# Optimization experiments

Hardware: AMD Instinct MI355X
Metric: run time of the kernel (lower is better)

Reference implementation:

```python
import jax, jax.numpy as jnp
import numpy as np

B, T, C = 2, 2048, 1024
H, D = 16, 64


def setup_inputs() -> dict:
    key = jax.random.key(0)
    ks = jax.random.split(key, 5)
    s = 1.0 / np.sqrt(C)  # keep projections well-scaled
    return {
        "x": jax.random.normal(ks[0], (B, T, C), dtype=jnp.float32),
        "wq": jax.random.normal(ks[1], (C, C), dtype=jnp.float32) * s,
        "wk": jax.random.normal(ks[2], (C, C), dtype=jnp.float32) * s,
        "wv": jax.random.normal(ks[3], (C, C), dtype=jnp.float32) * s,
        "wo": jax.random.normal(ks[4], (C, C), dtype=jnp.float32) * s,
    }


def reference(x, wq, wk, wv, wo):
    # nn.Linear(d,d,bias=False): y = x @ W.T ; weights stored [out,in]
    q = (x @ wq.T).reshape(B, T, H, D).transpose(0, 2, 1, 3)  # [B,H,T,D]
    k = (x @ wk.T).reshape(B, T, H, D).transpose(0, 2, 1, 3)
    v = (x @ wv.T).reshape(B, T, H, D).transpose(0, 2, 1, 3)
    scale = jnp.sqrt(jnp.float32(D))
    scores = jnp.einsum("bhtd,bhsd->bhts", q, k) / scale  # [B,H,T,T]
    # additive causal mask: -inf above the diagonal
    causal = jnp.tril(jnp.ones((T, T), dtype=bool))
    scores = jnp.where(causal[None, None], scores, jnp.float32(-1e9))
    weights = jax.nn.softmax(scores, axis=-1)
    out = jnp.einsum("bhts,bhsd->bhtd", weights, v)  # [B,H,T,D]
    out = out.transpose(0, 2, 1, 3).reshape(B, T, C)
    return out @ wo.T
```

## Files before the change

kernel.cpp:

```cpp
#include <hip/hip_runtime.h>
#include <stdint.h>

#define B_ 2
#define T_ 2048
#define C_ 1024
#define H_ 16
#define D_ 64
#define M_ (B_*T_)

typedef __attribute__((ext_vector_type(8))) short bf16x8;
typedef __attribute__((ext_vector_type(4))) short bf16x4;
typedef __attribute__((ext_vector_type(4))) float f32x4;
typedef unsigned short u16;

#define MFMA32(a, b, c) __builtin_amdgcn_mfma_f32_16x16x32_bf16((a), (b), (c), 0, 0, 0)
#if defined(__HIP_DEVICE_COMPILE__)
# if __has_builtin(__builtin_amdgcn_mfma_f32_16x16x16bf16_1k)
#  define MFMA16(a, b, c) __builtin_amdgcn_mfma_f32_16x16x16bf16_1k((a), (b), (c), 0, 0, 0)
# else
#  define MFMA16(a, b, c) __builtin_amdgcn_mfma_f32_16x16x16_bf16((a), (b), (c), 0, 0, 0)
# endif
#else
# define MFMA16(a, b, c) (c)
#endif

__device__ __forceinline__ u16 f2bf(float f) {
  union { float f; uint32_t u; } v; v.f = f;
  uint32_t u = v.u;
  return (u16)((u + 0x7fffu + ((u >> 16) & 1u)) >> 16);
}

__device__ __forceinline__ float exp2_fast(float x) { return __builtin_amdgcn_exp2f(x); }

typedef const __attribute__((address_space(1))) void* gas_t;
typedef __attribute__((address_space(3))) void* las_t;
__device__ __forceinline__ void gld_lds16(const void* g, void* l) {
  __builtin_amdgcn_global_load_lds((gas_t)g, (las_t)l, 16, 0, 0);
}

__global__ void cvt_bf16(const float* __restrict__ src, u16* __restrict__ dst) {
  int i = (blockIdx.x * blockDim.x + threadIdx.x) * 4;
  float4 v = *(const float4*)(src + i);
  ushort4 o;
  o.x = f2bf(v.x); o.y = f2bf(v.y); o.z = f2bf(v.z); o.w = f2bf(v.w);
  *(ushort4*)(dst + i) = o;
}

__global__ void cvt_bf16_w4(const float* __restrict__ s0, const float* __restrict__ s1,
                            const float* __restrict__ s2, const float* __restrict__ s3,
                            u16* __restrict__ d0, u16* __restrict__ d1,
                            u16* __restrict__ d2, u16* __restrict__ d3) {
  const float* s; u16* d;
  switch (blockIdx.y) {
    case 0: s = s0; d = d0; break;
    case 1: s = s1; d = d1; break;
    case 2: s = s2; d = d2; break;
    default: s = s3; d = d3; break;
  }
  int i = (blockIdx.x * blockDim.x + threadIdx.x) * 4;
  float4 v = *(const float4*)(s + i);
  ushort4 o;
  o.x = f2bf(v.x); o.y = f2bf(v.y); o.z = f2bf(v.z); o.w = f2bf(v.w);
  *(ushort4*)(d + i) = o;
}

__device__ __forceinline__ void gemm_core(const u16* __restrict__ A,
                                          const u16* __restrict__ W,
                                          int m0, int n0, int Kt,
                                          f32x4 acc[4][4])
{
  __shared__ u16 As[128*64];
  __shared__ u16 Bs[128*64];
  const int t = threadIdx.x;
  const int lane = t & 63;
  const int wave = t >> 6;
  const int q = lane >> 4;
  const int l15 = lane & 15;
  const int wm = (wave >> 1) * 64;
  const int wn = (wave & 1) * 64;

  #pragma unroll
  for (int i = 0; i < 4; ++i)
    #pragma unroll
    for (int j = 0; j < 4; ++j)
      acc[i][j] = (f32x4){0.f, 0.f, 0.f, 0.f};

  for (int k0 = 0; k0 < Kt; k0 += 64) {
    #pragma unroll
    for (int r = 0; r < 4; ++r) {
      int Lc = r * 256 + t;
      int row = Lc >> 3;
      int gcc = (Lc & 7) ^ (row & 7);
      gld_lds16(A + (size_t)(m0 + row) * Kt + k0 + gcc * 8, As + Lc * 8);
    }
    #pragma unroll
    for (int r = 0; r < 4; ++r) {
      int Lc = r * 256 + t;
      int row = Lc >> 3;
      int gcc = (Lc & 7) ^ (row & 7);
      gld_lds16(W + (size_t)(n0 + row) * Kt + k0 + gcc * 8, Bs + Lc * 8);
    }
    __syncthreads();

    #pragma unroll
    for (int kk = 0; kk < 2; ++kk) {
      bf16x8 af[4], bfr[4];
      #pragma unroll
      for (int i = 0; i < 4; ++i) {
        int m = wm + i * 16 + l15;
        int ch = (kk * 4 + q) ^ (m & 7);
        af[i] = *(const bf16x8*)(As + m * 64 + ch * 8);
      }
      #pragma unroll
      for (int j = 0; j < 4; ++j) {
        int n = wn + j * 16 + l15;
        int ch = (kk * 4 + q) ^ (n & 7);
        bfr[j] = *(const bf16x8*)(Bs + n * 64 + ch * 8);
      }
      #pragma unroll
      for (int i = 0; i < 4; ++i)
        #pragma unroll
        for (int j = 0; j < 4; ++j)
          acc[i][j] = MFMA32(af[i], bfr[j], acc[i][j]);
    }
    __syncthreads();
  }
}

#define QSCALE 0.1803368801111244f
__global__ __launch_bounds__(256, 3)
void gemm_qkv(const u16* __restrict__ X,
              const u16* __restrict__ Wq, const u16* __restrict__ Wk,
              const u16* __restrict__ Wv,
              u16* __restrict__ Q, u16* __restrict__ K, u16* __restrict__ Vt)
{
  const int bm = blockIdx.x;
  const int bn = blockIdx.y;
  const int seg = bn >> 3;
  const int n0 = (bn & 7) * 128;
  const u16* W = (seg == 0) ? Wq : ((seg == 1) ? Wk : Wv);

  f32x4 acc[4][4];
  gemm_core(X, W, bm * 128, n0, C_, acc);

  const int t = threadIdx.x, lane = t & 63, wave = t >> 6;
  const int q = lane >> 4, l15 = lane & 15;
  const int wm = (wave >> 1) * 64, wn = (wave & 1) * 64;
  const float scale = (seg == 0) ? QSCALE : 1.0f;

  #pragma unroll
  for (int i = 0; i < 4; ++i) {
    #pragma unroll
    for (int j = 0; j < 4; ++j) {
      const int mbase = bm * 128 + wm + i * 16 + q * 4;
      const int n = n0 + wn + j * 16 + l15;
      const int h = n >> 6, d = n & 63;
      if (seg < 2) {
        u16* dst = (seg == 0) ? Q : K;
        #pragma unroll
        for (int r = 0; r < 4; ++r) {
          const int m = mbase + r;
          const int b = m >> 11, tt = m & (T_ - 1);
          size_t idx = (((size_t)(b * H_ + h)) * T_ + tt) * D_ + d;
          dst[idx] = f2bf(acc[i][j][r] * scale);
        }
      } else {
        const int b = mbase >> 11, tt = mbase & (T_ - 1);
        size_t idx = (((size_t)(b * H_ + h)) * D_ + d) * T_ + tt;
        ushort4 pk;
        pk.x = f2bf(acc[i][j][0]); pk.y = f2bf(acc[i][j][1]);
        pk.z = f2bf(acc[i][j][2]); pk.w = f2bf(acc[i][j][3]);
        *(ushort4*)(Vt + idx) = pk;
      }
    }
  }
}

__global__ __launch_bounds__(256, 2)
void attn(const u16* __restrict__ Q, const u16* __restrict__ K,
          const u16* __restrict__ Vt, u16* __restrict__ Att)
{
  __shared__ u16 Ks[2][64 * 64];
  __shared__ u16 Vs[2][64 * 64];
  const int t = threadIdx.x;
  const int lane = t & 63, wave = t >> 6;
  const int q = lane >> 4, l15 = lane & 15;
  const int pr = blockIdx.x;
  const int bh = blockIdx.y;
  const int qbA = pr * 64;
  const int qbB = (31 - pr) * 64;
  const u16* Qp = Q + (size_t)bh * T_ * D_;
  const u16* Kp = K + (size_t)bh * T_ * D_;
  const u16* Vp = Vt + (size_t)bh * D_ * T_;

  const int rowA = qbA + 4 * l15 + wave;
  const int rowB = qbB + 4 * l15 + wave;
  const u16* qra = Qp + (size_t)rowA * 64;
  const u16* qrb = Qp + (size_t)rowB * 64;
  const bf16x8 aqA0 = *(const bf16x8*)(qra + q * 8);
  const bf16x8 aqA1 = *(const bf16x8*)(qra + 32 + q * 8);
  const bf16x8 aqB0 = *(const bf16x8*)(qrb + q * 8);
  const bf16x8 aqB1 = *(const bf16x8*)(qrb + 32 + q * 8);

  f32x4 oA[4], oB[4];
  #pragma unroll
  for (int j = 0; j < 4; ++j) {
    oA[j] = (f32x4){0.f, 0.f, 0.f, 0.f};
    oB[j] = (f32x4){0.f, 0.f, 0.f, 0.f};
  }
  float lsA = 0.f, lsB = 0.f;

  auto stage = [&](int kb, int buf) {
    #pragma unroll
    for (int r = 0; r < 2; ++r) {
      int c = r * 256 + t, row = c >> 3, gcc = (c & 7) ^ (row & 7);
      gld_lds16(Kp + (size_t)(kb + row) * 64 + gcc * 8, &Ks[buf][c * 8]);
    }
    #pragma unroll
    for (int r = 0; r < 2; ++r) {
      int c = r * 256 + t, row = c >> 3, gcc = (c & 7) ^ (row & 7);
      gld_lds16(Vp + (size_t)row * T_ + kb + gcc * 8, &Vs[buf][c * 8]);
    }
  };

  stage(0, 0);
  int cur = 0;
  for (int kb = 0; kb <= qbB; kb += 64, cur ^= 1) {
    __syncthreads();
    if (kb + 64 <= qbB) stage(kb + 64, cur ^ 1);
    const u16* Kc = &Ks[cur][0];
    const u16* Vc = &Vs[cur][0];

    bf16x8 kf0[4], kf1[4];
    #pragma unroll
    for (int j2 = 0; j2 < 4; ++j2) {
      const int row = j2 * 16 + l15;
      kf0[j2] = *(const bf16x8*)(Kc + row * 64 + ((q)     ^ (row & 7)) * 8);
      kf1[j2] = *(const bf16x8*)(Kc + row * 64 + ((4 + q) ^ (row & 7)) * 8);
    }
    bf16x4 vf[4][4];
    #pragma unroll
    for (int j = 0; j < 4; ++j) {
      const int row = j * 16 + l15;
      #pragma unroll
      for (int j2 = 0; j2 < 4; ++j2) {
        const int ch = (2 * j2 + (q >> 1)) ^ (row & 7);
        vf[j][j2] = *(const bf16x4*)(Vc + row * 64 + ch * 8 + (q & 1) * 4);
      }
    }

    auto tile_compute = [&](const bf16x8 a0, const bf16x8 a1, f32x4* o,
                            float& lsum, int rowg, bool diag) {
      bf16x4 pb[4];
      #pragma unroll
      for (int j2 = 0; j2 < 4; ++j2) {
        f32x4 z = (f32x4){0.f, 0.f, 0.f, 0.f};
        z = MFMA32(kf0[j2], a0, z);
        z = MFMA32(kf1[j2], a1, z);
        if (diag) {
          #pragma unroll
          for (int r = 0; r < 4; ++r) {
            const int key = kb + j2 * 16 + q * 4 + r;
            if (key > rowg) z[r] = -1e30f;
          }
        }
        float p0 = exp2_fast(z[0]), p1 = exp2_fast(z[1]);
        float p2 = exp2_fast(z[2]), p3 = exp2_fast(z[3]);
        lsum += (p0 + p1) + (p2 + p3);
        pb[j2] = (bf16x4){(short)f2bf(p0), (short)f2bf(p1),
                          (short)f2bf(p2), (short)f2bf(p3)};
      }
      #pragma unroll
      for (int j = 0; j < 4; ++j)
        #pragma unroll
        for (int j2 = 0; j2 < 4; ++j2)
          o[j] = MFMA16(vf[j][j2], pb[j2], o[j]);
    };

    tile_compute(aqB0, aqB1, oB, lsB, rowB, kb == qbB);
    if (kb <= qbA)
      tile_compute(aqA0, aqA1, oA, lsA, rowA, kb == qbA);
  }

  lsA += __shfl_xor(lsA, 16, 64); lsA += __shfl_xor(lsA, 32, 64);
  lsB += __shfl_xor(lsB, 16, 64); lsB += __shfl_xor(lsB, 32, 64);
  const float invA = __builtin_amdgcn_rcpf(lsA);
  const float invB = __builtin_amdgcn_rcpf(lsB);

  const int b = bh >> 4, h = bh & 15;
  #pragma unroll
  for (int j = 0; j < 4; ++j) {
    ushort4 pa, pbk;
    pa.x = f2bf(oA[j][0] * invA); pa.y = f2bf(oA[j][1] * invA);
    pa.z = f2bf(oA[j][2] * invA); pa.w = f2bf(oA[j][3] * invA);
    pbk.x = f2bf(oB[j][0] * invB); pbk.y = f2bf(oB[j][1] * invB);
    pbk.z = f2bf(oB[j][2] * invB); pbk.w = f2bf(oB[j][3] * invB);
    *(ushort4*)(Att + ((size_t)b * T_ + rowA) * C_ + h * 64 + j * 16 + q * 4) = pa;
    *(ushort4*)(Att + ((size_t)b * T_ + rowB) * C_ + h * 64 + j * 16 + q * 4) = pbk;
  }
}

__global__ __launch_bounds__(256, 3)
void gemm_out(const u16* __restrict__ Att, const u16* __restrict__ Wo,
              float* __restrict__ Out)
{
  const int bm = blockIdx.x, bn = blockIdx.y;
  f32x4 acc[4][4];
  gemm_core(Att, Wo, bm * 128, bn * 128, C_, acc);

  const int t = threadIdx.x, lane = t & 63, wave = t >> 6;
  const int q = lane >> 4, l15 = lane & 15;
  const int wm = (wave >> 1) * 64, wn = (wave & 1) * 64;

  #pragma unroll
  for (int i = 0; i < 4; ++i) {
    #pragma unroll
    for (int j = 0; j < 4; ++j) {
      const int m0 = bm * 128 + wm + i * 16 + q * 4;
      const int n = bn * 128 + wn + j * 16 + l15;
      #pragma unroll
      for (int r = 0; r < 4; ++r)
        Out[(size_t)(m0 + r) * C_ + n] = acc[i][j][r];
    }
  }
}

extern "C" void kernel_launch(void* const* d_in, const int* in_sizes, int n_in,
                              void* d_out, int out_size, void* d_ws, size_t ws_size,
                              hipStream_t stream) {
  const float* x  = (const float*)d_in[0];
  const float* wq = (const float*)d_in[1];
  const float* wk = (const float*)d_in[2];
  const float* wv = (const float*)d_in[3];
  const float* wo = (const float*)d_in[4];
  float* out = (float*)d_out;

  u16* ws  = (u16*)d_ws;
  u16* xb  = ws;
  u16* wqb = xb  + (size_t)M_ * C_;
  u16* wkb = wqb + (size_t)C_ * C_;
  u16* wvb = wkb + (size_t)C_ * C_;
  u16* wob = wvb + (size_t)C_ * C_;
  u16* Qb  = wob + (size_t)C_ * C_;
  u16* Kb  = Qb  + (size_t)M_ * C_;
  u16* Vtb = Kb  + (size_t)M_ * C_;
  u16* Atb = Vtb + (size_t)M_ * C_;

  cvt_bf16<<<dim3(M_ * C_ / 1024), 256, 0, stream>>>(x, xb);
  cvt_bf16_w4<<<dim3(C_ * C_ / 1024, 4), 256, 0, stream>>>(wq, wk, wv, wo,
                                                           wqb, wkb, wvb, wob);

  gemm_qkv<<<dim3(M_ / 128, 24), 256, 0, stream>>>(xb, wqb, wkb, wvb, Qb, Kb, Vtb);
  attn<<<dim3(16, B_ * H_), 256, 0, stream>>>(Qb, Kb, Vtb, Atb);
  gemm_out<<<dim3(M_ / 128, C_ / 128), 256, 0, stream>>>(Atb, wob, out);
}
```

Before: 176.8 us.

## Use 16x16x32 MFMA for PV via permuted V layout; retile output GEMM

The QKV GEMM now writes V transposed with a permuted token order inside each 32-token group. This lets the attention kernel load V as bf16x8 fragments and compute P·V with the 16x16x32 bf16 MFMA instead of pairs of 16x16x16 MFMAs, halving the PV instruction count and the number of LDS reads. The output projection gets its own kernel with 64x128 tiles, giving twice as many blocks so the GPU is better filled. That kernel is single-buffered, with a barrier on every k-step, which may expose load latency.

```diff
diff --git a/kernel.cpp b/kernel.cpp
--- a/kernel.cpp
+++ b/kernel.cpp
@@ -14,15 +14,6 @@
 typedef unsigned short u16;
 
 #define MFMA32(a, b, c) __builtin_amdgcn_mfma_f32_16x16x32_bf16((a), (b), (c), 0, 0, 0)
-#if defined(__HIP_DEVICE_COMPILE__)
-# if __has_builtin(__builtin_amdgcn_mfma_f32_16x16x16bf16_1k)
-#  define MFMA16(a, b, c) __builtin_amdgcn_mfma_f32_16x16x16bf16_1k((a), (b), (c), 0, 0, 0)
-# else
-#  define MFMA16(a, b, c) __builtin_amdgcn_mfma_f32_16x16x16_bf16((a), (b), (c), 0, 0, 0)
-# endif
-#else
-# define MFMA16(a, b, c) (c)
-#endif
 
 __device__ __forceinline__ u16 f2bf(float f) {
   union { float f; uint32_t u; } v; v.f = f;
@@ -166,7 +157,8 @@
         }
       } else {
         const int b = mbase >> 11, tt = mbase & (T_ - 1);
-        size_t idx = (((size_t)(b * H_ + h)) * D_ + d) * T_ + tt;
+        const int ttp = (tt & ~31) | ((tt & 12) << 1) | ((tt & 16) >> 2);
+        size_t idx = (((size_t)(b * H_ + h)) * D_ + d) * T_ + ttp;
         ushort4 pk;
         pk.x = f2bf(acc[i][j][0]); pk.y = f2bf(acc[i][j][1]);
         pk.z = f2bf(acc[i][j][2]); pk.w = f2bf(acc[i][j][3]);
@@ -238,14 +230,14 @@
       kf0[j2] = *(const bf16x8*)(Kc + row * 64 + ((q)     ^ (row & 7)) * 8);
       kf1[j2] = *(const bf16x8*)(Kc + row * 64 + ((4 + q) ^ (row & 7)) * 8);
     }
-    bf16x4 vf[4][4];
+    bf16x8 vfrag[4][2];
     #pragma unroll
     for (int j = 0; j < 4; ++j) {
       const int row = j * 16 + l15;
       #pragma unroll
-      for (int j2 = 0; j2 < 4; ++j2) {
-        const int ch = (2 * j2 + (q >> 1)) ^ (row & 7);
-        vf[j][j2] = *(const bf16x4*)(Vc + row * 64 + ch * 8 + (q & 1) * 4);
+      for (int kk = 0; kk < 2; ++kk) {
+        const int ch = (kk * 4 + q) ^ (row & 7);
+        vfrag[j][kk] = *(const bf16x8*)(Vc + row * 64 + ch * 8);
       }
     }
 
@@ -271,10 +263,13 @@
                           (short)f2bf(p2), (short)f2bf(p3)};
       }
       #pragma unroll
-      for (int j = 0; j < 4; ++j)
+      for (int kk = 0; kk < 2; ++kk) {
+        const bf16x8 pc = __builtin_shufflevector(pb[2 * kk], pb[2 * kk + 1],
+                                                  0, 1, 2, 3, 4, 5, 6, 7);
         #pragma unroll
-        for (int j2 = 0; j2 < 4; ++j2)
-          o[j] = MFMA16(vf[j][j2], pb[j2], o[j]);
+        for (int j = 0; j < 4; ++j)
+          o[j] = MFMA32(vfrag[j][kk], pc, o[j]);
+      }
     };
 
     tile_compute(aqB0, aqB1, oB, lsB, rowB, kb == qbB);
@@ -300,27 +295,71 @@
   }
 }
 
-__global__ __launch_bounds__(256, 3)
+__global__ __launch_bounds__(256, 2)
 void gemm_out(const u16* __restrict__ Att, const u16* __restrict__ Wo,
               float* __restrict__ Out)
 {
-  const int bm = blockIdx.x, bn = blockIdx.y;
-  f32x4 acc[4][4];
-  gemm_core(Att, Wo, bm * 128, bn * 128, C_, acc);
-
-  const int t = threadIdx.x, lane = t & 63, wave = t >> 6;
+  __shared__ u16 As[64 * 64];
+  __shared__ u16 Bs[128 * 64];
+  const int t = threadIdx.x;
+  const int lane = t & 63, wave = t >> 6;
   const int q = lane >> 4, l15 = lane & 15;
-  const int wm = (wave >> 1) * 64, wn = (wave & 1) * 64;
-
-  #pragma unroll
-  for (int i = 0; i < 4; ++i) {
+  const int wm = (wave >> 1) * 32, wn = (wave & 1) * 64;
+  const int m0 = blockIdx.x * 64, n0 = blockIdx.y * 128;
+
+  f32x4 acc[2][4];
+  #pragma unroll
+  for (int i = 0; i < 2; ++i)
+    #pragma unroll
+    for (int j = 0; j < 4; ++j)
+      acc[i][j] = (f32x4){0.f, 0.f, 0.f, 0.f};
+
+  for (int k0 = 0; k0 < C_; k0 += 64) {
+    #pragma unroll
+    for (int r = 0; r < 2; ++r) {
+      int Lc = r * 256 + t, row = Lc >> 3, gcc = (Lc & 7) ^ (row & 7);
+      gld_lds16(Att + (size_t)(m0 + row) * C_ + k0 + gcc * 8, As + Lc * 8);
+    }
+    #pragma unroll
+    for (int r = 0; r < 4; ++r) {
+      int Lc = r * 256 + t, row = Lc >> 3, gcc = (Lc & 7) ^ (row & 7);
+      gld_lds16(Wo + (size_t)(n0 + row) * C_ + k0 + gcc * 8, Bs + Lc * 8);
+    }
+    __syncthreads();
+
+    #pragma unroll
+    for (int kk = 0; kk < 2; ++kk) {
+      bf16x8 af[2], bfr[4];
+      #pragma unroll
+      for (int i = 0; i < 2; ++i) {
+        int m = wm + i * 16 + l15;
+        int ch = (kk * 4 + q) ^ (m & 7);
+        af[i] = *(const bf16x8*)(As + m * 64 + ch * 8);
+      }
+      #pragma unroll
+      for (int j = 0; j < 4; ++j) {
+        int n = wn + j * 16 + l15;
+        int ch = (kk * 4 + q) ^ (n & 7);
+        bfr[j] = *(const bf16x8*)(Bs + n * 64 + ch * 8);
+      }
+      #pragma unroll
+      for (int i = 0; i < 2; ++i)
+        #pragma unroll
+        for (int j = 0; j < 4; ++j)
+          acc[i][j] = MFMA32(af[i], bfr[j], acc[i][j]);
+    }
+    __syncthreads();
+  }
+
+  #pragma unroll
+  for (int i = 0; i < 2; ++i) {
     #pragma unroll
     for (int j = 0; j < 4; ++j) {
-      const int m0 = bm * 128 + wm + i * 16 + q * 4;
-      const int n = bn * 128 + wn + j * 16 + l15;
+      const int mm = m0 + wm + i * 16 + q * 4;
+      const int n = n0 + wn + j * 16 + l15;
       #pragma unroll
       for (int r = 0; r < 4; ++r)
-        Out[(size_t)(m0 + r) * C_ + n] = acc[i][j][r];
+        Out[(size_t)(mm + r) * C_ + n] = acc[i][j][r];
     }
   }
 }
@@ -352,5 +391,5 @@
 
   gemm_qkv<<<dim3(M_ / 128, 24), 256, 0, stream>>>(xb, wqb, wkb, wvb, Qb, Kb, Vtb);
   attn<<<dim3(16, B_ * H_), 256, 0, stream>>>(Qb, Kb, Vtb, Atb);
-  gemm_out<<<dim3(M_ / 128, C_ / 128), 256, 0, stream>>>(Atb, wob, out);
-}
+  gemm_out<<<dim3(M_ / 64, C_ / 128), 256, 0, stream>>>(Atb, wob, out);
+}
```

Result: faster. 171.8 us (-2.8%).
